# Optimization experiments

Hardware: AMD Instinct MI355X
Metric: run time of the kernel (lower is better)

## Reference

```python
import jax, jax.numpy as jnp
import numpy as np

N = 300_000
DEG = 16
E = N * DEG
EPS_W = 1e-12  # guard for zero-distance neighbors
EPS_A = 1e-8   # diagonal regularization of the 3x3 normal matrix


def setup_inputs() -> dict:
    key = jax.random.key(0)
    k1, k2, k3 = jax.random.split(key, 3)
    coordinates = jax.random.normal(k1, (N, 3), dtype=jnp.float32)
    u = jax.random.normal(k2, (N, 1), dtype=jnp.float32)
    # uniform-degree CSR: offsets[i] = i*DEG
    offsets = (jnp.arange(N + 1) * DEG).astype(jnp.int32)
    indices = jax.random.randint(k3, (E,), 0, N, dtype=jnp.int32)
    return {"coordinates": coordinates, "u": u, "offsets": offsets, "indices": indices}


def _mesh_lsq_gradient(coords, values, offsets, indices):
    """Weighted least-squares gradient reconstruction over a CSR neighbor list.

    coords: [N,3], values: [N,C], offsets: [N+1], indices: [E].
    Returns [N,3,C]: per-node gradient of each channel.
    """
    n = coords.shape[0]
    e = indices.shape[0]
    # node id owning each edge: offsets[i] <= e < offsets[i+1]
    seg = jnp.searchsorted(offsets, jnp.arange(e, dtype=offsets.dtype), side='right') - 1
    dx = coords[indices] - coords[seg]            # [E,3]
    dv = values[indices] - values[seg]            # [E,C]
    w = 1.0 / jnp.maximum(jnp.sum(dx * dx, axis=-1), EPS_W)  # inverse-distance^2 weights [E]
    # normal equations: A g = b per node
    A = jax.ops.segment_sum(w[:, None, None] * dx[:, :, None] * dx[:, None, :], seg, num_segments=n)  # [N,3,3]
    b = jax.ops.segment_sum(w[:, None, None] * dx[:, :, None] * dv[:, None, :], seg, num_segments=n)  # [N,3,C]
    A = A + EPS_A * jnp.eye(3, dtype=coords.dtype)
    return jnp.linalg.solve(A, b)  # [N,3,C]


def reference(coordinates, u, offsets, indices):
    coords = jax.lax.stop_gradient(coordinates)  # original does coords.detach()
    vals = u[:, 0:1]                              # squeeze(-1), keep as 1 channel
    first = _mesh_lsq_gradient(coords, vals, offsets, indices)[..., 0]   # [N,3] = (u_x,u_y,u_z)
    # second pass: gradients of all three first derivatives at once (channels)
    second = _mesh_lsq_gradient(coords, first, offsets, indices)         # [N,3,3]; second[:,b,a] = d(du/dx_a)/dx_b
    u_xx = second[:, 0, 0]
    u_yy = second[:, 1, 1]
    u_zz = second[:, 2, 2]
    u_xy = second[:, 1, 0]  # mixed = second_grads[a][:, b] for a<b
    u_xz = second[:, 2, 0]
    u_yz = second[:, 2, 1]
    # columns: [xx, yy, zz, xy, xz, yz] (mixed derivs returned once; module duplicates symmetric keys)
    return jnp.stack([u_xx, u_yy, u_zz, u_xy, u_xz, u_yz], axis=-1)
```

## Files before the change

### kernel.cpp

```cpp
#include <hip/hip_runtime.h>
#include <hip/hip_fp16.h>


constexpr int N_NODES = 300000;
constexpr int DEG = 16;
constexpr float EPS_W = 1e-12f;
constexpr double EPS_A = 1e-8;

typedef float        f32x4 __attribute__((ext_vector_type(4)));
typedef float        f32x2 __attribute__((ext_vector_type(2)));
typedef int          i32x4 __attribute__((ext_vector_type(4)));
typedef unsigned int u32x4 __attribute__((ext_vector_type(4)));
typedef unsigned int u32x2 __attribute__((ext_vector_type(2)));

__device__ __forceinline__ float redux4(float v) {
    v += __shfl_xor(v, 1, 4);
    v += __shfl_xor(v, 2, 4);
    return v;
}

__device__ __forceinline__ unsigned int pack_h2(float a, float b) {
    union { __half2 h2; unsigned int ui; } pk;
    pk.h2 = __halves2half2(__float2half_rn(a), __float2half_rn(b));
    return pk.ui;
}

__device__ __forceinline__ f32x2 unpack_h2(unsigned int v) {
    union { __half2 h2; unsigned int ui; } pk;
    pk.ui = v;
    f32x2 r = { __low2float(pk.h2), __high2float(pk.h2) };
    return r;
}

__global__ __launch_bounds__(256) void pack_p1(
    const float* __restrict__ coords,
    const float* __restrict__ u,
    float4* __restrict__ p1)
{
    int i = blockIdx.x * 256 + threadIdx.x;
    if (i >= N_NODES) return;
    p1[i] = make_float4(coords[3 * i], coords[3 * i + 1],
                        coords[3 * i + 2], u[i]);
}

__global__ __launch_bounds__(256) void lsq_pass1(
    const float4*  __restrict__ P,
    const int*     __restrict__ indices,
    u32x2*         __restrict__ Gh,
    f32x4*         __restrict__ M,
    unsigned int*  __restrict__ WXY,
    unsigned int*  __restrict__ WZ)
{
    int tid  = blockIdx.x * 256 + threadIdx.x;
    int node = tid >> 2;
    int q    = tid & 3;
    if (node >= N_NODES) return;

    float4 c = P[node];
    int ebase = node * DEG + q * 4;
    i32x4 idx = __builtin_nontemporal_load((const i32x4*)(indices + ebase));

    float4 n0 = P[idx.x];
    float4 n1 = P[idx.y];
    float4 n2 = P[idx.z];
    float4 n3 = P[idx.w];

    float a00 = 0, a01 = 0, a02 = 0, a11 = 0, a12 = 0, a22 = 0;
    float b0 = 0, b1 = 0, b2 = 0;
    float wxs[4], wys[4], wzs[4];
    float4 nb[4] = {n0, n1, n2, n3};
    #pragma unroll
    for (int k = 0; k < 4; ++k) {
        float dx = nb[k].x - c.x, dy = nb[k].y - c.y;
        float dz = nb[k].z - c.z, dv = nb[k].w - c.w;
        float w = 1.0f / fmaxf(dx * dx + dy * dy + dz * dz, EPS_W);
        float wx = w * dx, wy = w * dy, wz = w * dz;
        wxs[k] = wx; wys[k] = wy; wzs[k] = wz;
        a00 += wx * dx; a01 += wx * dy; a02 += wx * dz;
        a11 += wy * dy; a12 += wy * dz; a22 += wz * dz;
        b0 += wx * dv; b1 += wy * dv; b2 += wz * dv;
    }

    u32x4 wxy = { pack_h2(wxs[0], wys[0]), pack_h2(wxs[1], wys[1]),
                  pack_h2(wxs[2], wys[2]), pack_h2(wxs[3], wys[3]) };
    __builtin_nontemporal_store(wxy, (u32x4*)(WXY + ebase));
    u32x2 wzp = { pack_h2(wzs[0], wzs[1]), pack_h2(wzs[2], wzs[3]) };
    __builtin_nontemporal_store(wzp, (u32x2*)(WZ + (ebase >> 1)));

    a00 = redux4(a00); a01 = redux4(a01); a02 = redux4(a02);
    a11 = redux4(a11); a12 = redux4(a12); a22 = redux4(a22);
    b0 = redux4(b0); b1 = redux4(b1); b2 = redux4(b2);

    if (q == 0) {
        double A00 = (double)a00 + EPS_A;
        double A11 = (double)a11 + EPS_A;
        double A22 = (double)a22 + EPS_A;
        double A01 = (double)a01, A02 = (double)a02, A12 = (double)a12;
        double j00 = A11 * A22 - A12 * A12;
        double j01 = A02 * A12 - A01 * A22;
        double j02 = A01 * A12 - A02 * A11;
        double j11 = A00 * A22 - A02 * A02;
        double j12 = A01 * A02 - A00 * A12;
        double j22 = A00 * A11 - A01 * A01;
        double det = A00 * j00 + A01 * j01 + A02 * j02;
        double inv = 1.0 / det;
        float m00 = (float)(j00 * inv), m01 = (float)(j01 * inv);
        float m02 = (float)(j02 * inv), m11 = (float)(j11 * inv);
        float m12 = (float)(j12 * inv), m22 = (float)(j22 * inv);
        float g0 = m00 * b0 + m01 * b1 + m02 * b2;
        float g1 = m01 * b0 + m11 * b1 + m12 * b2;
        float g2 = m02 * b0 + m12 * b1 + m22 * b2;
        u32x2 gp = { pack_h2(g0, g1), pack_h2(g2, 0.0f) };
        Gh[node] = gp;
        f32x4 mv0 = {m00, m01, m02, m11};
        f32x4 mv1 = {m12, m22, 0.0f, 0.0f};
        __builtin_nontemporal_store(mv0, M + 2 * node);
        __builtin_nontemporal_store(mv1, M + 2 * node + 1);
    }
}

__global__ __launch_bounds__(256) void lsq_pass2(
    const u32x2*        __restrict__ Gh,
    const f32x4*        __restrict__ M,
    const unsigned int* __restrict__ WXY,
    const unsigned int* __restrict__ WZ,
    const int*          __restrict__ indices,
    float*              __restrict__ out)
{
    int tid  = blockIdx.x * 256 + threadIdx.x;
    int node = tid >> 2;
    int q    = tid & 3;
    if (node >= N_NODES) return;

    u32x2 gip = Gh[node];
    f32x2 gi01 = unpack_h2(gip.x);
    f32x2 gi2_ = unpack_h2(gip.y);
    float gi0 = gi01.x, gi1 = gi01.y, gi2 = gi2_.x;

    int ebase = node * DEG + q * 4;
    i32x4 idx = __builtin_nontemporal_load((const i32x4*)(indices + ebase));
    u32x4 wxy = __builtin_nontemporal_load((const u32x4*)(WXY + ebase));
    u32x2 wzp = __builtin_nontemporal_load((const u32x2*)(WZ + (ebase >> 1)));

    u32x2 gp0 = Gh[idx.x];
    u32x2 gp1 = Gh[idx.y];
    u32x2 gp2 = Gh[idx.z];
    u32x2 gp3 = Gh[idx.w];

    float b00 = 0, b10 = 0, b20 = 0;
    float b01 = 0, b11 = 0, b21 = 0;
    float b02 = 0, b12 = 0, b22 = 0;
    u32x2 gb[4] = {gp0, gp1, gp2, gp3};
    unsigned int wzs[2] = {wzp.x, wzp.y};
    unsigned int wxys[4] = {wxy.x, wxy.y, wxy.z, wxy.w};
    #pragma unroll
    for (int k = 0; k < 4; ++k) {
        f32x2 wxyf = unpack_h2(wxys[k]);
        float wx = wxyf.x, wy = wxyf.y;
        f32x2 wzf = unpack_h2(wzs[k >> 1]);
        float wz = (k & 1) ? wzf.y : wzf.x;
        f32x2 gj01 = unpack_h2(gb[k].x);
        f32x2 gj2_ = unpack_h2(gb[k].y);
        float dv0 = gj01.x - gi0, dv1 = gj01.y - gi1, dv2 = gj2_.x - gi2;
        b00 += wx * dv0; b10 += wy * dv0; b20 += wz * dv0;
        b01 += wx * dv1; b11 += wy * dv1; b21 += wz * dv1;
        b02 += wx * dv2; b12 += wy * dv2; b22 += wz * dv2;
    }

    b00 = redux4(b00); b10 = redux4(b10); b20 = redux4(b20);
    b01 = redux4(b01); b11 = redux4(b11); b21 = redux4(b21);
    b02 = redux4(b02); b12 = redux4(b12); b22 = redux4(b22);

    if (q == 0) {
        f32x4 m0 = __builtin_nontemporal_load(M + 2 * node);
        f32x4 m1 = __builtin_nontemporal_load(M + 2 * node + 1);
        float m00 = m0.x, m01 = m0.y, m02 = m0.z, m11 = m0.w;
        float m12 = m1.x, m22 = m1.y;
        float x00 = m00 * b00 + m01 * b10 + m02 * b20;
        float x10 = m01 * b00 + m11 * b10 + m12 * b20;
        float x20 = m02 * b00 + m12 * b10 + m22 * b20;
        float x11 = m01 * b01 + m11 * b11 + m12 * b21;
        float x21 = m02 * b01 + m12 * b11 + m22 * b21;
        float x22 = m02 * b02 + m12 * b12 + m22 * b22;
        f32x2* o2 = (f32x2*)(out + 6 * node);
        f32x2 o0 = {x00, x11};
        f32x2 o1 = {x22, x10};
        f32x2 o2v = {x20, x21};
        __builtin_nontemporal_store(o0,  o2 + 0);
        __builtin_nontemporal_store(o1,  o2 + 1);
        __builtin_nontemporal_store(o2v, o2 + 2);
    }
}

extern "C" void kernel_launch(void* const* d_in, const int* in_sizes, int n_in,
                              void* d_out, int out_size, void* d_ws, size_t ws_size,
                              hipStream_t stream) {
    const float* coords  = (const float*)d_in[0];
    const float* u       = (const float*)d_in[1];
    const int*   indices = (const int*)d_in[3];
    float*       out     = (float*)d_out;

    char* ws = (char*)d_ws;
    const size_t szP1  = (size_t)N_NODES * 16;
    const size_t szGh  = (size_t)N_NODES * 8;
    const size_t szM   = (size_t)N_NODES * 32;
    const size_t szWXY = (size_t)N_NODES * DEG * 4;

    float4*       P1  = (float4*)ws;
    u32x2*        Gh  = (u32x2*)(ws + szP1);
    f32x4*        M   = (f32x4*)(ws + szP1 + szGh);
    unsigned int* WXY = (unsigned int*)(ws + szP1 + szGh + szM);
    unsigned int* WZ  = (unsigned int*)(ws + szP1 + szGh + szM + szWXY);

    const int block = 256;
    const int grid_nodes = (N_NODES + block - 1) / block;
    const int threads4 = N_NODES * 4;
    const int grid4 = (threads4 + block - 1) / block;

    pack_p1<<<grid_nodes, block, 0, stream>>>(coords, u, P1);
    lsq_pass1<<<grid4, block, 0, stream>>>(P1, indices, Gh, M, WXY, WZ);
    lsq_pass2<<<grid4, block, 0, stream>>>(Gh, M, WXY, WZ, indices, out);
}
```

Before: 144.7 us.

## Process each node with two lanes of eight edges and split M storage

Both LSQ passes now give each node 2 threads handling 8 edges apiece instead of 4 threads handling 4 edges. This halves the shuffle reduction depth and the idle lanes in the per-node solve, and raises memory-level parallelism per thread through 8 outstanding gathers. The inverse-matrix workspace is split into a 16-byte and an 8-byte array, dropping the padded 32-byte layout to cut write and read traffic. In exchange there are fewer total threads and higher register use per thread, which may lower occupancy.

```diff
diff --git a/kernel.cpp b/kernel.cpp
--- a/kernel.cpp
+++ b/kernel.cpp
@@ -13,10 +13,8 @@
 typedef unsigned int u32x4 __attribute__((ext_vector_type(4)));
 typedef unsigned int u32x2 __attribute__((ext_vector_type(2)));
 
-__device__ __forceinline__ float redux4(float v) {
-    v += __shfl_xor(v, 1, 4);
-    v += __shfl_xor(v, 2, 4);
-    return v;
+__device__ __forceinline__ float redux2(float v) {
+    return v + __shfl_xor(v, 1, 2);
 }
 
 __device__ __forceinline__ unsigned int pack_h2(float a, float b) {
@@ -47,30 +45,30 @@
     const float4*  __restrict__ P,
     const int*     __restrict__ indices,
     u32x2*         __restrict__ Gh,
-    f32x4*         __restrict__ M,
+    f32x4*         __restrict__ M0,
+    f32x2*         __restrict__ M1,
     unsigned int*  __restrict__ WXY,
     unsigned int*  __restrict__ WZ)
 {
     int tid  = blockIdx.x * 256 + threadIdx.x;
-    int node = tid >> 2;
-    int q    = tid & 3;
+    int node = tid >> 1;
+    int h    = tid & 1;
     if (node >= N_NODES) return;
 
     float4 c = P[node];
-    int ebase = node * DEG + q * 4;
-    i32x4 idx = __builtin_nontemporal_load((const i32x4*)(indices + ebase));
-
-    float4 n0 = P[idx.x];
-    float4 n1 = P[idx.y];
-    float4 n2 = P[idx.z];
-    float4 n3 = P[idx.w];
+    int ebase = node * DEG + h * 8;
+    i32x4 ia = __builtin_nontemporal_load((const i32x4*)(indices + ebase));
+    i32x4 ib = __builtin_nontemporal_load((const i32x4*)(indices + ebase + 4));
+
+    float4 nb[8];
+    nb[0] = P[ia.x]; nb[1] = P[ia.y]; nb[2] = P[ia.z]; nb[3] = P[ia.w];
+    nb[4] = P[ib.x]; nb[5] = P[ib.y]; nb[6] = P[ib.z]; nb[7] = P[ib.w];
 
     float a00 = 0, a01 = 0, a02 = 0, a11 = 0, a12 = 0, a22 = 0;
     float b0 = 0, b1 = 0, b2 = 0;
-    float wxs[4], wys[4], wzs[4];
-    float4 nb[4] = {n0, n1, n2, n3};
+    float wxs[8], wys[8], wzs[8];
     #pragma unroll
-    for (int k = 0; k < 4; ++k) {
+    for (int k = 0; k < 8; ++k) {
         float dx = nb[k].x - c.x, dy = nb[k].y - c.y;
         float dz = nb[k].z - c.z, dv = nb[k].w - c.w;
         float w = 1.0f / fmaxf(dx * dx + dy * dy + dz * dz, EPS_W);
@@ -81,17 +79,21 @@
         b0 += wx * dv; b1 += wy * dv; b2 += wz * dv;
     }
 
-    u32x4 wxy = { pack_h2(wxs[0], wys[0]), pack_h2(wxs[1], wys[1]),
-                  pack_h2(wxs[2], wys[2]), pack_h2(wxs[3], wys[3]) };
-    __builtin_nontemporal_store(wxy, (u32x4*)(WXY + ebase));
-    u32x2 wzp = { pack_h2(wzs[0], wzs[1]), pack_h2(wzs[2], wzs[3]) };
-    __builtin_nontemporal_store(wzp, (u32x2*)(WZ + (ebase >> 1)));
-
-    a00 = redux4(a00); a01 = redux4(a01); a02 = redux4(a02);
-    a11 = redux4(a11); a12 = redux4(a12); a22 = redux4(a22);
-    b0 = redux4(b0); b1 = redux4(b1); b2 = redux4(b2);
-
-    if (q == 0) {
+    u32x4 wxyA = { pack_h2(wxs[0], wys[0]), pack_h2(wxs[1], wys[1]),
+                   pack_h2(wxs[2], wys[2]), pack_h2(wxs[3], wys[3]) };
+    u32x4 wxyB = { pack_h2(wxs[4], wys[4]), pack_h2(wxs[5], wys[5]),
+                   pack_h2(wxs[6], wys[6]), pack_h2(wxs[7], wys[7]) };
+    __builtin_nontemporal_store(wxyA, (u32x4*)(WXY + ebase));
+    __builtin_nontemporal_store(wxyB, (u32x4*)(WXY + ebase + 4));
+    u32x4 wzp = { pack_h2(wzs[0], wzs[1]), pack_h2(wzs[2], wzs[3]),
+                  pack_h2(wzs[4], wzs[5]), pack_h2(wzs[6], wzs[7]) };
+    __builtin_nontemporal_store(wzp, (u32x4*)(WZ + (ebase >> 1)));
+
+    a00 = redux2(a00); a01 = redux2(a01); a02 = redux2(a02);
+    a11 = redux2(a11); a12 = redux2(a12); a22 = redux2(a22);
+    b0 = redux2(b0); b1 = redux2(b1); b2 = redux2(b2);
+
+    if (h == 0) {
         double A00 = (double)a00 + EPS_A;
         double A11 = (double)a11 + EPS_A;
         double A22 = (double)a22 + EPS_A;
@@ -113,23 +115,24 @@
         u32x2 gp = { pack_h2(g0, g1), pack_h2(g2, 0.0f) };
         Gh[node] = gp;
         f32x4 mv0 = {m00, m01, m02, m11};
-        f32x4 mv1 = {m12, m22, 0.0f, 0.0f};
-        __builtin_nontemporal_store(mv0, M + 2 * node);
-        __builtin_nontemporal_store(mv1, M + 2 * node + 1);
+        f32x2 mv1 = {m12, m22};
+        __builtin_nontemporal_store(mv0, M0 + node);
+        __builtin_nontemporal_store(mv1, M1 + node);
     }
 }
 
 __global__ __launch_bounds__(256) void lsq_pass2(
     const u32x2*        __restrict__ Gh,
-    const f32x4*        __restrict__ M,
+    const f32x4*        __restrict__ M0,
+    const f32x2*        __restrict__ M1,
     const unsigned int* __restrict__ WXY,
     const unsigned int* __restrict__ WZ,
     const int*          __restrict__ indices,
     float*              __restrict__ out)
 {
     int tid  = blockIdx.x * 256 + threadIdx.x;
-    int node = tid >> 2;
-    int q    = tid & 3;
+    int node = tid >> 1;
+    int h    = tid & 1;
     if (node >= N_NODES) return;
 
     u32x2 gip = Gh[node];
@@ -137,27 +140,28 @@
     f32x2 gi2_ = unpack_h2(gip.y);
     float gi0 = gi01.x, gi1 = gi01.y, gi2 = gi2_.x;
 
-    int ebase = node * DEG + q * 4;
-    i32x4 idx = __builtin_nontemporal_load((const i32x4*)(indices + ebase));
-    u32x4 wxy = __builtin_nontemporal_load((const u32x4*)(WXY + ebase));
-    u32x2 wzp = __builtin_nontemporal_load((const u32x2*)(WZ + (ebase >> 1)));
-
-    u32x2 gp0 = Gh[idx.x];
-    u32x2 gp1 = Gh[idx.y];
-    u32x2 gp2 = Gh[idx.z];
-    u32x2 gp3 = Gh[idx.w];
+    int ebase = node * DEG + h * 8;
+    i32x4 ia = __builtin_nontemporal_load((const i32x4*)(indices + ebase));
+    i32x4 ib = __builtin_nontemporal_load((const i32x4*)(indices + ebase + 4));
+    u32x4 wxyA = __builtin_nontemporal_load((const u32x4*)(WXY + ebase));
+    u32x4 wxyB = __builtin_nontemporal_load((const u32x4*)(WXY + ebase + 4));
+    u32x4 wzp  = __builtin_nontemporal_load((const u32x4*)(WZ + (ebase >> 1)));
+
+    u32x2 gb[8];
+    gb[0] = Gh[ia.x]; gb[1] = Gh[ia.y]; gb[2] = Gh[ia.z]; gb[3] = Gh[ia.w];
+    gb[4] = Gh[ib.x]; gb[5] = Gh[ib.y]; gb[6] = Gh[ib.z]; gb[7] = Gh[ib.w];
 
     float b00 = 0, b10 = 0, b20 = 0;
     float b01 = 0, b11 = 0, b21 = 0;
     float b02 = 0, b12 = 0, b22 = 0;
-    u32x2 gb[4] = {gp0, gp1, gp2, gp3};
-    unsigned int wzs[2] = {wzp.x, wzp.y};
-    unsigned int wxys[4] = {wxy.x, wxy.y, wxy.z, wxy.w};
+    unsigned int wxys[8] = {wxyA.x, wxyA.y, wxyA.z, wxyA.w,
+                            wxyB.x, wxyB.y, wxyB.z, wxyB.w};
+    unsigned int wzs[4] = {wzp.x, wzp.y, wzp.z, wzp.w};
     #pragma unroll
-    for (int k = 0; k < 4; ++k) {
+    for (int k = 0; k < 8; ++k) {
         f32x2 wxyf = unpack_h2(wxys[k]);
+        f32x2 wzf  = unpack_h2(wzs[k >> 1]);
         float wx = wxyf.x, wy = wxyf.y;
-        f32x2 wzf = unpack_h2(wzs[k >> 1]);
         float wz = (k & 1) ? wzf.y : wzf.x;
         f32x2 gj01 = unpack_h2(gb[k].x);
         f32x2 gj2_ = unpack_h2(gb[k].y);
@@ -167,13 +171,13 @@
         b02 += wx * dv2; b12 += wy * dv2; b22 += wz * dv2;
     }
 
-    b00 = redux4(b00); b10 = redux4(b10); b20 = redux4(b20);
-    b01 = redux4(b01); b11 = redux4(b11); b21 = redux4(b21);
-    b02 = redux4(b02); b12 = redux4(b12); b22 = redux4(b22);
-
-    if (q == 0) {
-        f32x4 m0 = __builtin_nontemporal_load(M + 2 * node);
-        f32x4 m1 = __builtin_nontemporal_load(M + 2 * node + 1);
+    b00 = redux2(b00); b10 = redux2(b10); b20 = redux2(b20);
+    b01 = redux2(b01); b11 = redux2(b11); b21 = redux2(b21);
+    b02 = redux2(b02); b12 = redux2(b12); b22 = redux2(b22);
+
+    if (h == 0) {
+        f32x4 m0 = __builtin_nontemporal_load(M0 + node);
+        f32x2 m1 = __builtin_nontemporal_load(M1 + node);
         float m00 = m0.x, m01 = m0.y, m02 = m0.z, m11 = m0.w;
         float m12 = m1.x, m22 = m1.y;
         float x00 = m00 * b00 + m01 * b10 + m02 * b20;
@@ -203,21 +207,23 @@
     char* ws = (char*)d_ws;
     const size_t szP1  = (size_t)N_NODES * 16;
     const size_t szGh  = (size_t)N_NODES * 8;
-    const size_t szM   = (size_t)N_NODES * 32;
+    const size_t szM0  = (size_t)N_NODES * 16;
+    const size_t szM1  = (size_t)N_NODES * 8;
     const size_t szWXY = (size_t)N_NODES * DEG * 4;
 
     float4*       P1  = (float4*)ws;
     u32x2*        Gh  = (u32x2*)(ws + szP1);
-    f32x4*        M   = (f32x4*)(ws + szP1 + szGh);
-    unsigned int* WXY = (unsigned int*)(ws + szP1 + szGh + szM);
-    unsigned int* WZ  = (unsigned int*)(ws + szP1 + szGh + szM + szWXY);
+    f32x4*        M0  = (f32x4*)(ws + szP1 + szGh);
+    f32x2*        M1  = (f32x2*)(ws + szP1 + szGh + szM0);
+    unsigned int* WXY = (unsigned int*)(ws + szP1 + szGh + szM0 + szM1);
+    unsigned int* WZ  = (unsigned int*)(ws + szP1 + szGh + szM0 + szM1 + szWXY);
 
     const int block = 256;
     const int grid_nodes = (N_NODES + block - 1) / block;
-    const int threads4 = N_NODES * 4;
-    const int grid4 = (threads4 + block - 1) / block;
+    const int threads2 = N_NODES * 2;
+    const int grid2 = (threads2 + block - 1) / block;
 
     pack_p1<<<grid_nodes, block, 0, stream>>>(coords, u, P1);
-    lsq_pass1<<<grid4, block, 0, stream>>>(P1, indices, Gh, M, WXY, WZ);
-    lsq_pass2<<<grid4, block, 0, stream>>>(Gh, M, WXY, WZ, indices, out);
-}
+    lsq_pass1<<<grid2, block, 0, stream>>>(P1, indices, Gh, M0, M1, WXY, WZ);
+    lsq_pass2<<<grid2, block, 0, stream>>>(Gh, M0, M1, WXY, WZ, indices, out);
+}
```

Result: slower. 148.2 us (+2.4%).
